# Kernel optimization log

Hardware: AMD Instinct MI355X
Metric: run time of the kernel (lower is better)

The kernel has to match this reference:

```python
import jax, jax.numpy as jnp
import numpy as np

N = 100000   # nodes
E = 640000   # edges (before self-loops)
G = 1000     # graphs in batch
D_IN = 100
D = 128
EPS = 1e-5


def setup_inputs() -> dict:
    key = jax.random.key(0)
    ks = jax.random.split(key, 12)
    x = jax.random.normal(ks[0], (N, D_IN), dtype=jnp.float32)
    edge_index = jax.random.randint(ks[1], (2, E), 0, N, dtype=jnp.int64)
    edge_weight = jax.random.uniform(ks[2], (E,), dtype=jnp.float32)
    batch = jnp.sort(jax.random.randint(ks[3], (N,), 0, G, dtype=jnp.int64))
    def glorot(k, shape):
        fan = shape[0]
        return jax.random.normal(k, shape, dtype=jnp.float32) / np.float32(np.sqrt(fan))
    return {
        "x": x, "edge_index": edge_index, "edge_weight": edge_weight, "batch": batch,
        "W0": glorot(ks[4], (D_IN, D)), "b0": jnp.zeros((D,), jnp.float32),
        "W1": glorot(ks[5], (D, D)),    "b1": jnp.zeros((D,), jnp.float32),
        "W2": glorot(ks[6], (D, D)),    "b2": jnp.zeros((D,), jnp.float32),
        "gamma": jnp.ones((3, D), jnp.float32), "beta": jnp.zeros((3, D), jnp.float32),
        "run_mean": jnp.zeros((3, D), jnp.float32), "run_var": jnp.ones((3, D), jnp.float32),
        "Wout": glorot(ks[7], (D, 1)), "bout": jnp.zeros((1,), jnp.float32),
    }


def reference(x, edge_index, edge_weight, batch, W0, b0, W1, b1, W2, b2,
              gamma, beta, run_mean, run_var, Wout, bout):
    n = x.shape[0]
    # add self-loops with weight 1 (GCNConv default)
    loop = jnp.arange(n, dtype=edge_index.dtype)
    src = jnp.concatenate([edge_index[0], loop])
    dst = jnp.concatenate([edge_index[1], loop])
    ew = jnp.concatenate([edge_weight, jnp.ones((n,), edge_weight.dtype)])
    # symmetric normalization: D^{-1/2} A D^{-1/2}
    deg = jax.ops.segment_sum(ew, dst, num_segments=n)
    dinv = jnp.where(deg > 0, jax.lax.rsqrt(deg), 0.0)
    norm = dinv[src] * ew * dinv[dst]            # [E+N]

    def gcn_bn_relu(h, W, b, g, bt, rm, rv):
        h = h @ W                                 # linear first (cheaper gather dim)
        agg = jax.ops.segment_sum(h[src] * norm[:, None], dst, num_segments=n)
        agg = agg + b
        # BatchNorm1d in eval mode (running stats); dropout is identity in eval
        agg = g * (agg - rm) * jax.lax.rsqrt(rv + EPS) + bt
        return jax.nn.relu(agg)

    h = gcn_bn_relu(x, W0, b0, gamma[0], beta[0], run_mean[0], run_var[0])
    h = gcn_bn_relu(h, W1, b1, gamma[1], beta[1], run_mean[1], run_var[1])
    h = gcn_bn_relu(h, W2, b2, gamma[2], beta[2], run_mean[2], run_var[2])

    # global mean pool over graphs
    counts = jax.ops.segment_sum(jnp.ones((n,), h.dtype), batch, num_segments=G)
    pooled = jax.ops.segment_sum(h, batch, num_segments=G) / jnp.maximum(counts, 1.0)[:, None]
    return pooled @ Wout + bout
```

## Files before the change

### kernel.cpp

```cpp
#include <hip/hip_runtime.h>

#define BN_EPS 1e-5f
#define BINCAP 32

static inline size_t align_up(size_t x, size_t a) { return (x + a - 1) & ~(a - 1); }

typedef __attribute__((ext_vector_type(8))) short bf16x8;
typedef __attribute__((ext_vector_type(4))) float f32x4;

__device__ __forceinline__ void bf16split(float v, unsigned short& hi, unsigned short& lo) {
    unsigned u = __float_as_uint(v);
    unsigned rh = (u + 0x7FFFu + ((u >> 16) & 1u)) >> 16;
    float fh = __uint_as_float(rh << 16);
    hi = (unsigned short)rh;
    float rem = v - fh;
    unsigned u2 = __float_as_uint(rem);
    lo = (unsigned short)((u2 + 0x7FFFu + ((u2 >> 16) & 1u)) >> 16);
}

__device__ __forceinline__ unsigned short bf16rne(float v) {
    unsigned u = __float_as_uint(v);
    return (unsigned short)((u + 0x7FFFu + ((u >> 16) & 1u)) >> 16);
}

__device__ __forceinline__ float bf16f(unsigned h) { return __uint_as_float(h << 16); }
__device__ __forceinline__ float chlo(unsigned u) { return __uint_as_float(u << 16); }
__device__ __forceinline__ float chhi(unsigned u) { return __uint_as_float(u & 0xffff0000u); }


__global__ void place_kernel(const int* __restrict__ src, const int* __restrict__ dst,
                             const float* __restrict__ ew,
                             int* __restrict__ cntc, int2* __restrict__ bins, int E) {
    int e = blockIdx.x * blockDim.x + threadIdx.x;
    if (e >= E) return;
    int d = dst[e];
    int pos = atomicAdd(&cntc[d], 1);
    if (pos < BINCAP)
        bins[(size_t)d * BINCAP + pos] = make_int2(src[e], __float_as_int(ew[e]));
}


__global__ void deginv_kernel(const int* __restrict__ cntc, const int2* __restrict__ bins,
                              float* __restrict__ dinv, int N) {
    int i = blockIdx.x * blockDim.x + threadIdx.x;
    if (i >= N) return;
    int cnt = cntc[i]; if (cnt > BINCAP) cnt = BINCAP;
    const int2* b = bins + (size_t)i * BINCAP;
    float s = 0.f;
    for (int j = 0; j < cnt; ++j) s += __int_as_float(b[j].y);
    dinv[i] = rsqrtf(s + 1.0f);
}


__global__ void normfix_kernel(const int* __restrict__ cntc, int2* __restrict__ bins,
                               const float* __restrict__ dinv, int N) {
    int i = blockIdx.x * blockDim.x + threadIdx.x;
    if (i >= N) return;
    int cnt = cntc[i]; if (cnt > BINCAP) cnt = BINCAP;
    float di = dinv[i];
    int2* b = bins + (size_t)i * BINCAP;
    for (int j = 0; j < cnt; ++j) {
        int2 pr = b[j];
        float w = __int_as_float(pr.y) * dinv[pr.x] * di;
        b[j].y = __float_as_int(w);
    }
}


__global__ void convw_kernel(const float* __restrict__ W0, const float* __restrict__ W1,
                             const float* __restrict__ W2, int K0,
                             unsigned short* __restrict__ Whi, unsigned short* __restrict__ Wlo) {
    int idx = blockIdx.x * blockDim.x + threadIdx.x;
    if (idx >= 3 * 32 * 64 * 8) return;
    int j    = idx & 7;
    int lane = (idx >> 3) & 63;
    int f    = (idx >> 9) & 31;
    int l    = idx >> 14;
    int ct = f >> 2, k0c = f & 3;
    int quad = lane >> 4, m16 = lane & 15;
    int n = ct * 16 + m16;
    int k = k0c * 32 + quad * 8 + j;
    const float* W = (l == 0) ? W0 : (l == 1) ? W1 : W2;
    int Kl = (l == 0) ? K0 : 128;
    float v = (k < Kl) ? W[(size_t)k * 128 + n] : 0.f;
    unsigned short hi, lo;
    bf16split(v, hi, lo);
    Whi[idx] = hi;
    Wlo[idx] = lo;
}


__device__ __forceinline__ void mfma_tail(const bf16x8 ah[4], const bf16x8 al[4],
                                          const unsigned short* __restrict__ Whi,
                                          const unsigned short* __restrict__ Wlo,
                                          unsigned short* __restrict__ Yh,
                                          int row0, int quad, int m16, int lane, int N) {
    const bf16x8* Wh8 = (const bf16x8*)Whi;
    const bf16x8* Wl8 = (const bf16x8*)Wlo;

    f32x4 acc[8];
    #pragma unroll
    for (int ct = 0; ct < 8; ++ct) acc[ct] = (f32x4){0.f, 0.f, 0.f, 0.f};

    bf16x8 bh[2][4], bl[2][4];
    #pragma unroll
    for (int k0c = 0; k0c < 4; ++k0c) {
        bh[0][k0c] = Wh8[k0c * 64 + lane];
        bl[0][k0c] = Wl8[k0c * 64 + lane];
    }

    __builtin_amdgcn_s_setprio(1);
    #pragma unroll
    for (int ct = 0; ct < 8; ++ct) {
        int cur = ct & 1, nxt = cur ^ 1;
        if (ct < 7) {
            #pragma unroll
            for (int k0c = 0; k0c < 4; ++k0c) {
                bh[nxt][k0c] = Wh8[((ct + 1) * 4 + k0c) * 64 + lane];
                bl[nxt][k0c] = Wl8[((ct + 1) * 4 + k0c) * 64 + lane];
            }
        }
        #pragma unroll
        for (int k0c = 0; k0c < 4; ++k0c) {
            acc[ct] = __builtin_amdgcn_mfma_f32_16x16x32_bf16(ah[k0c], bh[cur][k0c], acc[ct], 0, 0, 0);
            acc[ct] = __builtin_amdgcn_mfma_f32_16x16x32_bf16(ah[k0c], bl[cur][k0c], acc[ct], 0, 0, 0);
            acc[ct] = __builtin_amdgcn_mfma_f32_16x16x32_bf16(al[k0c], bh[cur][k0c], acc[ct], 0, 0, 0);
        }
    }
    __builtin_amdgcn_s_setprio(0);

    #pragma unroll
    for (int ct = 0; ct < 8; ++ct) {
        #pragma unroll
        for (int rg = 0; rg < 4; ++rg) {
            int row = row0 + quad * 4 + rg;
            if (row < N)
                Yh[(size_t)row * 128 + ct * 16 + m16] = bf16rne(acc[ct][rg]);
        }
    }
}


__launch_bounds__(256, 2)
__global__ void gemm0_fused_kernel(const float* __restrict__ x, int D_IN,
                                   const unsigned short* __restrict__ Whi,
                                   const unsigned short* __restrict__ Wlo,
                                   unsigned short* __restrict__ Yh, int N) {
    int tid = threadIdx.x;
    int wid = tid >> 6, lane = tid & 63;
    int quad = lane >> 4, m16 = lane & 15;
    int row0 = blockIdx.x * 64 + wid * 16;

    int arow = row0 + m16;
    if (arow > N - 1) arow = N - 1;
    const float* xr = x + (size_t)arow * D_IN;

    bf16x8 ah[4], al[4];
    #pragma unroll
    for (int k0c = 0; k0c < 4; ++k0c) {
        int kb = k0c * 32 + quad * 8;
        float vs[8];
        if (kb + 8 <= D_IN) {
            float4 v0 = *((const float4*)(xr + kb));
            float4 v1 = *((const float4*)(xr + kb + 4));
            vs[0] = v0.x; vs[1] = v0.y; vs[2] = v0.z; vs[3] = v0.w;
            vs[4] = v1.x; vs[5] = v1.y; vs[6] = v1.z; vs[7] = v1.w;
        } else {
            #pragma unroll
            for (int j = 0; j < 8; ++j) vs[j] = (kb + j < D_IN) ? xr[kb + j] : 0.f;
        }
        #pragma unroll
        for (int j = 0; j < 8; ++j) {
            unsigned short hi, lo;
            bf16split(vs[j], hi, lo);
            ah[k0c][j] = (short)hi;
            al[k0c][j] = (short)lo;
        }
    }

    mfma_tail(ah, al, Whi, Wlo, Yh, row0, quad, m16, lane, N);
}


__global__ void scaleshift_kernel(const float* __restrict__ gamma, const float* __restrict__ beta,
                                  const float* __restrict__ rm, const float* __restrict__ rv,
                                  const float* __restrict__ b0, const float* __restrict__ b1,
                                  const float* __restrict__ b2,
                                  float* __restrict__ scale, float* __restrict__ shift) {
    int t = threadIdx.x;
    int l = t >> 7, j = t & 127;
    const float* bs = (l == 0) ? b0 : (l == 1) ? b1 : b2;
    float sc = gamma[t] * rsqrtf(rv[t] + BN_EPS);
    scale[t] = sc;
    shift[t] = beta[t] + (bs[j] - rm[t]) * sc;
}


__device__ __forceinline__ void gather_pair(const unsigned* __restrict__ Yh32,
                                            int2 pr0, int m0, int2 pr1, int m1,
                                            int lane,
                                            float& ax0, float& ay0, float& ax1, float& ay1) {
    int mr0 = (m0 + 7) & ~7, mr1 = (m1 + 7) & ~7;
    int mr = mr0 > mr1 ? mr0 : mr1;
    for (int j = 0; j < mr; j += 8) {
        int a0 = __builtin_amdgcn_readlane(pr0.x, j);
        int a1 = __builtin_amdgcn_readlane(pr0.x, j + 1);
        int a2 = __builtin_amdgcn_readlane(pr0.x, j + 2);
        int a3 = __builtin_amdgcn_readlane(pr0.x, j + 3);
        int a4 = __builtin_amdgcn_readlane(pr0.x, j + 4);
        int a5 = __builtin_amdgcn_readlane(pr0.x, j + 5);
        int a6 = __builtin_amdgcn_readlane(pr0.x, j + 6);
        int a7 = __builtin_amdgcn_readlane(pr0.x, j + 7);
        int b0 = __builtin_amdgcn_readlane(pr1.x, j);
        int b1 = __builtin_amdgcn_readlane(pr1.x, j + 1);
        int b2 = __builtin_amdgcn_readlane(pr1.x, j + 2);
        int b3 = __builtin_amdgcn_readlane(pr1.x, j + 3);
        int b4 = __builtin_amdgcn_readlane(pr1.x, j + 4);
        int b5 = __builtin_amdgcn_readlane(pr1.x, j + 5);
        int b6 = __builtin_amdgcn_readlane(pr1.x, j + 6);
        int b7 = __builtin_amdgcn_readlane(pr1.x, j + 7);
        float wa0 = __int_as_float(__builtin_amdgcn_readlane(pr0.y, j));
        float wa1 = __int_as_float(__builtin_amdgcn_readlane(pr0.y, j + 1));
        float wa2 = __int_as_float(__builtin_amdgcn_readlane(pr0.y, j + 2));
        float wa3 = __int_as_float(__builtin_amdgcn_readlane(pr0.y, j + 3));
        float wa4 = __int_as_float(__builtin_amdgcn_readlane(pr0.y, j + 4));
        float wa5 = __int_as_float(__builtin_amdgcn_readlane(pr0.y, j + 5));
        float wa6 = __int_as_float(__builtin_amdgcn_readlane(pr0.y, j + 6));
        float wa7 = __int_as_float(__builtin_amdgcn_readlane(pr0.y, j + 7));
        float wb0 = __int_as_float(__builtin_amdgcn_readlane(pr1.y, j));
        float wb1 = __int_as_float(__builtin_amdgcn_readlane(pr1.y, j + 1));
        float wb2 = __int_as_float(__builtin_amdgcn_readlane(pr1.y, j + 2));
        float wb3 = __int_as_float(__builtin_amdgcn_readlane(pr1.y, j + 3));
        float wb4 = __int_as_float(__builtin_amdgcn_readlane(pr1.y, j + 4));
        float wb5 = __int_as_float(__builtin_amdgcn_readlane(pr1.y, j + 5));
        float wb6 = __int_as_float(__builtin_amdgcn_readlane(pr1.y, j + 6));
        float wb7 = __int_as_float(__builtin_amdgcn_readlane(pr1.y, j + 7));
        unsigned ua0 = Yh32[(size_t)a0 * 64 + lane];
        unsigned ua1 = Yh32[(size_t)a1 * 64 + lane];
        unsigned ua2 = Yh32[(size_t)a2 * 64 + lane];
        unsigned ua3 = Yh32[(size_t)a3 * 64 + lane];
        unsigned ua4 = Yh32[(size_t)a4 * 64 + lane];
        unsigned ua5 = Yh32[(size_t)a5 * 64 + lane];
        unsigned ua6 = Yh32[(size_t)a6 * 64 + lane];
        unsigned ua7 = Yh32[(size_t)a7 * 64 + lane];
        unsigned ub0 = Yh32[(size_t)b0 * 64 + lane];
        unsigned ub1 = Yh32[(size_t)b1 * 64 + lane];
        unsigned ub2 = Yh32[(size_t)b2 * 64 + lane];
        unsigned ub3 = Yh32[(size_t)b3 * 64 + lane];
        unsigned ub4 = Yh32[(size_t)b4 * 64 + lane];
        unsigned ub5 = Yh32[(size_t)b5 * 64 + lane];
        unsigned ub6 = Yh32[(size_t)b6 * 64 + lane];
        unsigned ub7 = Yh32[(size_t)b7 * 64 + lane];
        ax0 += chlo(ua0) * wa0; ay0 += chhi(ua0) * wa0;
        ax0 += chlo(ua1) * wa1; ay0 += chhi(ua1) * wa1;
        ax0 += chlo(ua2) * wa2; ay0 += chhi(ua2) * wa2;
        ax0 += chlo(ua3) * wa3; ay0 += chhi(ua3) * wa3;
        ax0 += chlo(ua4) * wa4; ay0 += chhi(ua4) * wa4;
        ax0 += chlo(ua5) * wa5; ay0 += chhi(ua5) * wa5;
        ax0 += chlo(ua6) * wa6; ay0 += chhi(ua6) * wa6;
        ax0 += chlo(ua7) * wa7; ay0 += chhi(ua7) * wa7;
        ax1 += chlo(ub0) * wb0; ay1 += chhi(ub0) * wb0;
        ax1 += chlo(ub1) * wb1; ay1 += chhi(ub1) * wb1;
        ax1 += chlo(ub2) * wb2; ay1 += chhi(ub2) * wb2;
        ax1 += chlo(ub3) * wb3; ay1 += chhi(ub3) * wb3;
        ax1 += chlo(ub4) * wb4; ay1 += chhi(ub4) * wb4;
        ax1 += chlo(ub5) * wb5; ay1 += chhi(ub5) * wb5;
        ax1 += chlo(ub6) * wb6; ay1 += chhi(ub6) * wb6;
        ax1 += chlo(ub7) * wb7; ay1 += chhi(ub7) * wb7;
    }
}


__launch_bounds__(64, 4)
__global__ void fused_agg_gemm_kernel(
        const unsigned* __restrict__ Yh_in,
        const int2* __restrict__ bins, const int* __restrict__ cntc,
        const float* __restrict__ dinv,
        const float* __restrict__ scale, const float* __restrict__ shift,
        const unsigned short* __restrict__ Whi, const unsigned short* __restrict__ Wlo,
        unsigned short* __restrict__ Yh_out, int N) {
    __shared__ float sA[16 * 132];
    int lane = threadIdx.x;
    int quad = lane >> 4, m16 = lane & 15;
    int row0 = blockIdx.x * 16;

    float2 sc = ((const float2*)scale)[lane];
    float2 sh = ((const float2*)shift)[lane];

    int mm[16]; float dv[16]; unsigned uh[16]; int2 gg[16];
    #pragma unroll
    for (int i = 0; i < 16; ++i) {
        int n = row0 + i; if (n > N - 1) n = N - 1;
        mm[i] = cntc[n];
        dv[i] = dinv[n];
        uh[i] = Yh_in[(size_t)n * 64 + lane];
    }
    #pragma unroll
    for (int i = 0; i < 16; ++i) {
        int n = row0 + i; if (n > N - 1) n = N - 1;
        int m = mm[i]; if (m > BINCAP) m = BINCAP;
        mm[i] = m;
        gg[i] = (lane < m) ? bins[(size_t)n * BINCAP + lane] : make_int2(n, 0);
    }

    #pragma unroll
    for (int i = 0; i < 16; i += 2) {
        float w00 = dv[i] * dv[i], w01 = dv[i + 1] * dv[i + 1];
        float ax0 = chlo(uh[i]) * w00,     ay0 = chhi(uh[i]) * w00;
        float ax1 = chlo(uh[i + 1]) * w01, ay1 = chhi(uh[i + 1]) * w01;
        gather_pair(Yh_in, gg[i], mm[i], gg[i + 1], mm[i + 1], lane, ax0, ay0, ax1, ay1);
        float ox0 = fmaxf(ax0 * sc.x + sh.x, 0.f);
        float oy0 = fmaxf(ay0 * sc.y + sh.y, 0.f);
        float ox1 = fmaxf(ax1 * sc.x + sh.x, 0.f);
        float oy1 = fmaxf(ay1 * sc.y + sh.y, 0.f);
        *((float2*)&sA[i * 132 + 2 * lane])       = make_float2(ox0, oy0);
        *((float2*)&sA[(i + 1) * 132 + 2 * lane]) = make_float2(ox1, oy1);
    }

    asm volatile("s_waitcnt lgkmcnt(0)" ::: "memory");
    __builtin_amdgcn_sched_barrier(0);

    bf16x8 ah[4], al[4];
    #pragma unroll
    for (int k0c = 0; k0c < 4; ++k0c) {
        float4 v0 = *((const float4*)&sA[m16 * 132 + k0c * 32 + quad * 8]);
        float4 v1 = *((const float4*)&sA[m16 * 132 + k0c * 32 + quad * 8 + 4]);
        float vs[8] = {v0.x, v0.y, v0.z, v0.w, v1.x, v1.y, v1.z, v1.w};
        #pragma unroll
        for (int j = 0; j < 8; ++j) {
            unsigned short hi, lo;
            bf16split(vs[j], hi, lo);
            ah[k0c][j] = (short)hi;
            al[k0c][j] = (short)lo;
        }
    }

    mfma_tail(ah, al, Whi, Wlo, Yh_out, row0, quad, m16, lane, N);
}


__launch_bounds__(256)
__global__ void agg3_kernel(const unsigned* __restrict__ Yh32,
                            const int2* __restrict__ bins, const int* __restrict__ cntc,
                            const float* __restrict__ dinv,
                            const float* __restrict__ scale, const float* __restrict__ shift,
                            const float* __restrict__ Wout,
                            float* __restrict__ snode, int N) {
    int idx = blockIdx.x * blockDim.x + threadIdx.x;
    int pairid = idx >> 6, lane = idx & 63;
    int n0 = pairid * 2;
    if (n0 >= N) return;
    int n1 = n0 + 1; if (n1 > N - 1) n1 = n0;

    int m0 = cntc[n0];
    int m1 = cntc[n1];
    float d0 = dinv[n0], d1 = dinv[n1];
    unsigned uh0 = Yh32[(size_t)n0 * 64 + lane];
    unsigned uh1 = Yh32[(size_t)n1 * 64 + lane];
    if (m0 > BINCAP) m0 = BINCAP;
    if (m1 > BINCAP) m1 = BINCAP;
    int2 pr0 = (lane < m0) ? bins[(size_t)n0 * BINCAP + lane] : make_int2(n0, 0);
    int2 pr1 = (lane < m1) ? bins[(size_t)n1 * BINCAP + lane] : make_int2(n1, 0);

    float w00 = d0 * d0, w01 = d1 * d1;
    float ax0 = chlo(uh0) * w00, ay0 = chhi(uh0) * w00;
    float ax1 = chlo(uh1) * w01, ay1 = chhi(uh1) * w01;
    gather_pair(Yh32, pr0, m0, pr1, m1, lane, ax0, ay0, ax1, ay1);

    float2 sc = ((const float2*)scale)[lane];
    float2 sh = ((const float2*)shift)[lane];
    float2 w  = ((const float2*)Wout)[lane];
    float ox0 = fmaxf(ax0 * sc.x + sh.x, 0.f);
    float oy0 = fmaxf(ay0 * sc.y + sh.y, 0.f);
    float ox1 = fmaxf(ax1 * sc.x + sh.x, 0.f);
    float oy1 = fmaxf(ay1 * sc.y + sh.y, 0.f);
    float s0 = ox0 * w.x + oy0 * w.y;
    float s1 = ox1 * w.x + oy1 * w.y;
    #pragma unroll
    for (int off = 32; off > 0; off >>= 1) {
        s0 += __shfl_down(s0, off, 64);
        s1 += __shfl_down(s1, off, 64);
    }
    if (lane == 0) {
        snode[n0] = s0;
        if (n1 != n0) snode[n1] = s1;
    }
}


__global__ void bounds_kernel(const int* __restrict__ batch, int* __restrict__ gstart,
                              int N, int G) {
    int i = blockIdx.x * blockDim.x + threadIdx.x;
    if (i >= N) return;
    int b = batch[i];
    int prev = (i == 0) ? -1 : batch[i - 1];
    for (int g = prev + 1; g <= b; ++g) gstart[g] = i;
    if (i == N - 1) {
        for (int g = b + 1; g <= G; ++g) gstart[g] = N;
    }
}

__launch_bounds__(256)
__global__ void pool3_kernel(const float* __restrict__ snode, const int* __restrict__ gstart,
                             const float* __restrict__ bout, float* __restrict__ out, int G) {
    int g = blockIdx.x;
    int beg = gstart[g], end = gstart[g + 1];
    int t = threadIdx.x;
    float acc = 0.f;
    for (int n = beg + t; n < end; n += 256) acc += snode[n];
    __shared__ float lds[256];
    lds[t] = acc;
    __syncthreads();
    if (t < 64) lds[t] = lds[t] + lds[t + 64] + lds[t + 128] + lds[t + 192];
    __syncthreads();
    if (t < 64) {
        float s = lds[t];
        #pragma unroll
        for (int off = 32; off > 0; off >>= 1) s += __shfl_down(s, off, 64);
        if (t == 0) {
            float cntf = (float)(end - beg);
            out[g] = s / fmaxf(cntf, 1.0f) + bout[0];
        }
    }
}


extern "C" void kernel_launch(void* const* d_in, const int* in_sizes, int n_in,
                              void* d_out, int out_size, void* d_ws, size_t ws_size,
                              hipStream_t stream) {
    const float* x     = (const float*)d_in[0];
    const int*   ei    = (const int*)d_in[1];
    const float* ew    = (const float*)d_in[2];
    const int*   batch = (const int*)d_in[3];
    const float* W0 = (const float*)d_in[4];
    const float* b0 = (const float*)d_in[5];
    const float* W1 = (const float*)d_in[6];
    const float* b1 = (const float*)d_in[7];
    const float* W2 = (const float*)d_in[8];
    const float* b2 = (const float*)d_in[9];
    const float* gamma = (const float*)d_in[10];
    const float* beta  = (const float*)d_in[11];
    const float* rmean = (const float*)d_in[12];
    const float* rvar  = (const float*)d_in[13];
    const float* Wout  = (const float*)d_in[14];
    const float* bout  = (const float*)d_in[15];

    const int E = in_sizes[2];
    const int N = in_sizes[3];
    const int D_IN = in_sizes[0] / N;
    const int G = out_size;

    const int* src = ei;
    const int* dst = ei + E;

    char* ws = (char*)d_ws;
    size_t off = 0;
    float* dinv  = (float*)(ws + off); off = align_up(off + (size_t)N * 4, 256);
    int* cntc    = (int*)(ws + off);   off = align_up(off + (size_t)N * 4, 256);
    int* gstart  = (int*)(ws + off);   off = align_up(off + ((size_t)G + 1) * 4, 256);
    int2* bins   = (int2*)(ws + off);  off = align_up(off + (size_t)N * BINCAP * 8, 256);
    unsigned short* YAh = (unsigned short*)(ws + off); off = align_up(off + (size_t)N * 128 * 2, 256);
    unsigned short* YBh = (unsigned short*)(ws + off); off = align_up(off + (size_t)N * 128 * 2, 256);
    unsigned short* Whi = (unsigned short*)(ws + off); off = align_up(off + 3 * 16384 * 2, 256);
    unsigned short* Wlo = (unsigned short*)(ws + off); off = align_up(off + 3 * 16384 * 2, 256);
    float* scale = (float*)(ws + off); off = align_up(off + 3 * 128 * 4, 256);
    float* shift = (float*)(ws + off); off = align_up(off + 3 * 128 * 4, 256);
    float* snode = (float*)(ws + off); off = align_up(off + (size_t)N * 4, 256);
    (void)ws_size;

    hipMemsetAsync(cntc, 0, (size_t)N * 4, stream);

    const int tB = 256;
    place_kernel<<<(E + tB - 1) / tB, tB, 0, stream>>>(src, dst, ew, cntc, bins, E);
    deginv_kernel<<<(N + tB - 1) / tB, tB, 0, stream>>>(cntc, bins, dinv, N);
    normfix_kernel<<<(N + tB - 1) / tB, tB, 0, stream>>>(cntc, bins, dinv, N);
    bounds_kernel<<<(N + tB - 1) / tB, tB, 0, stream>>>(batch, gstart, N, G);
    scaleshift_kernel<<<1, 384, 0, stream>>>(gamma, beta, rmean, rvar, b0, b1, b2, scale, shift);
    convw_kernel<<<(3 * 32 * 64 * 8 + tB - 1) / tB, tB, 0, stream>>>(W0, W1, W2, D_IN, Whi, Wlo);

    int gemm0_blocks = (N + 63) / 64;
    int fused_blocks = (N + 15) / 16;

    gemm0_fused_kernel<<<gemm0_blocks, 256, 0, stream>>>(x, D_IN, Whi, Wlo, YAh, N);
    fused_agg_gemm_kernel<<<fused_blocks, 64, 0, stream>>>(
        (const unsigned*)YAh, bins, cntc, dinv,
        scale, shift, Whi + 16384, Wlo + 16384, YBh, N);
    fused_agg_gemm_kernel<<<fused_blocks, 64, 0, stream>>>(
        (const unsigned*)YBh, bins, cntc, dinv,
        scale + 128, shift + 128, Whi + 2 * 16384, Wlo + 2 * 16384, YAh, N);
    {
        long nthread_pair = (long)((N + 1) / 2) * 64;
        int blocks_pair = (int)((nthread_pair + tB - 1) / tB);
        agg3_kernel<<<blocks_pair, tB, 0, stream>>>((const unsigned*)YAh,
            bins, cntc, dinv, scale + 256, shift + 256, Wout, snode, N);
    }

    pool3_kernel<<<G, 256, 0, stream>>>(snode, gstart, bout, (float*)d_out, G);
}
```

Baseline: 318.7 us.

## Merge prep kernels and software-pipeline neighbor gathers in fused aggregation

Combines the weight conversion, BN scale/shift and graph-bounds kernels into one launch to cut launch overhead. In the fused aggregation+GEMM kernel, the first eight neighbor loads plus the self row for the next node pair are issued while the current pair accumulates, double-buffering gathered values to hide memory latency. The extra buffered registers may lower occupancy, and gather_pair is refactored into loops.

```diff
diff --git a/kernel.cpp b/kernel.cpp
--- a/kernel.cpp
+++ b/kernel.cpp
@@ -23,9 +23,9 @@
     return (unsigned short)((u + 0x7FFFu + ((u >> 16) & 1u)) >> 16);
 }
 
-__device__ __forceinline__ float bf16f(unsigned h) { return __uint_as_float(h << 16); }
 __device__ __forceinline__ float chlo(unsigned u) { return __uint_as_float(u << 16); }
 __device__ __forceinline__ float chhi(unsigned u) { return __uint_as_float(u & 0xffff0000u); }
+
 
 
 __global__ void place_kernel(const int* __restrict__ src, const int* __restrict__ dst,
@@ -67,26 +67,50 @@
 }
 
 
-__global__ void convw_kernel(const float* __restrict__ W0, const float* __restrict__ W1,
-                             const float* __restrict__ W2, int K0,
-                             unsigned short* __restrict__ Whi, unsigned short* __restrict__ Wlo) {
+__global__ void prep_kernel(const float* __restrict__ W0, const float* __restrict__ W1,
+                            const float* __restrict__ W2, int K0,
+                            unsigned short* __restrict__ Whi, unsigned short* __restrict__ Wlo,
+                            const float* __restrict__ gamma, const float* __restrict__ beta,
+                            const float* __restrict__ rm, const float* __restrict__ rv,
+                            const float* __restrict__ b0, const float* __restrict__ b1,
+                            const float* __restrict__ b2,
+                            float* __restrict__ scale, float* __restrict__ shift,
+                            const int* __restrict__ batch, int* __restrict__ gstart,
+                            int N, int G) {
     int idx = blockIdx.x * blockDim.x + threadIdx.x;
-    if (idx >= 3 * 32 * 64 * 8) return;
-    int j    = idx & 7;
-    int lane = (idx >> 3) & 63;
-    int f    = (idx >> 9) & 31;
-    int l    = idx >> 14;
-    int ct = f >> 2, k0c = f & 3;
-    int quad = lane >> 4, m16 = lane & 15;
-    int n = ct * 16 + m16;
-    int k = k0c * 32 + quad * 8 + j;
-    const float* W = (l == 0) ? W0 : (l == 1) ? W1 : W2;
-    int Kl = (l == 0) ? K0 : 128;
-    float v = (k < Kl) ? W[(size_t)k * 128 + n] : 0.f;
-    unsigned short hi, lo;
-    bf16split(v, hi, lo);
-    Whi[idx] = hi;
-    Wlo[idx] = lo;
+    if (idx < 3 * 32 * 64 * 8) {
+        int j    = idx & 7;
+        int lane = (idx >> 3) & 63;
+        int f    = (idx >> 9) & 31;
+        int l    = idx >> 14;
+        int ct = f >> 2, k0c = f & 3;
+        int quad = lane >> 4, m16 = lane & 15;
+        int n = ct * 16 + m16;
+        int k = k0c * 32 + quad * 8 + j;
+        const float* W = (l == 0) ? W0 : (l == 1) ? W1 : W2;
+        int Kl = (l == 0) ? K0 : 128;
+        float v = (k < Kl) ? W[(size_t)k * 128 + n] : 0.f;
+        unsigned short hi, lo;
+        bf16split(v, hi, lo);
+        Whi[idx] = hi;
+        Wlo[idx] = lo;
+    } else if (idx < 3 * 32 * 64 * 8 + 384) {
+        int t = idx - 3 * 32 * 64 * 8;
+        int l = t >> 7, j = t & 127;
+        const float* bs = (l == 0) ? b0 : (l == 1) ? b1 : b2;
+        float sc = gamma[t] * rsqrtf(rv[t] + BN_EPS);
+        scale[t] = sc;
+        shift[t] = beta[t] + (bs[j] - rm[t]) * sc;
+    } else {
+        int i = idx - (3 * 32 * 64 * 8 + 384);
+        if (i >= N) return;
+        int b = batch[i];
+        int prev = (i == 0) ? -1 : batch[i - 1];
+        for (int g = prev + 1; g <= b; ++g) gstart[g] = i;
+        if (i == N - 1) {
+            for (int g = b + 1; g <= G; ++g) gstart[g] = N;
+        }
+    }
 }
 
 
@@ -182,20 +206,6 @@
 }
 
 
-__global__ void scaleshift_kernel(const float* __restrict__ gamma, const float* __restrict__ beta,
-                                  const float* __restrict__ rm, const float* __restrict__ rv,
-                                  const float* __restrict__ b0, const float* __restrict__ b1,
-                                  const float* __restrict__ b2,
-                                  float* __restrict__ scale, float* __restrict__ shift) {
-    int t = threadIdx.x;
-    int l = t >> 7, j = t & 127;
-    const float* bs = (l == 0) ? b0 : (l == 1) ? b1 : b2;
-    float sc = gamma[t] * rsqrtf(rv[t] + BN_EPS);
-    scale[t] = sc;
-    shift[t] = beta[t] + (bs[j] - rm[t]) * sc;
-}
-
-
 __device__ __forceinline__ void gather_pair(const unsigned* __restrict__ Yh32,
                                             int2 pr0, int m0, int2 pr1, int m1,
                                             int lane,
@@ -203,70 +213,21 @@
     int mr0 = (m0 + 7) & ~7, mr1 = (m1 + 7) & ~7;
     int mr = mr0 > mr1 ? mr0 : mr1;
     for (int j = 0; j < mr; j += 8) {
-        int a0 = __builtin_amdgcn_readlane(pr0.x, j);
-        int a1 = __builtin_amdgcn_readlane(pr0.x, j + 1);
-        int a2 = __builtin_amdgcn_readlane(pr0.x, j + 2);
-        int a3 = __builtin_amdgcn_readlane(pr0.x, j + 3);
-        int a4 = __builtin_amdgcn_readlane(pr0.x, j + 4);
-        int a5 = __builtin_amdgcn_readlane(pr0.x, j + 5);
-        int a6 = __builtin_amdgcn_readlane(pr0.x, j + 6);
-        int a7 = __builtin_amdgcn_readlane(pr0.x, j + 7);
-        int b0 = __builtin_amdgcn_readlane(pr1.x, j);
-        int b1 = __builtin_amdgcn_readlane(pr1.x, j + 1);
-        int b2 = __builtin_amdgcn_readlane(pr1.x, j + 2);
-        int b3 = __builtin_amdgcn_readlane(pr1.x, j + 3);
-        int b4 = __builtin_amdgcn_readlane(pr1.x, j + 4);
-        int b5 = __builtin_amdgcn_readlane(pr1.x, j + 5);
-        int b6 = __builtin_amdgcn_readlane(pr1.x, j + 6);
-        int b7 = __builtin_amdgcn_readlane(pr1.x, j + 7);
-        float wa0 = __int_as_float(__builtin_amdgcn_readlane(pr0.y, j));
-        float wa1 = __int_as_float(__builtin_amdgcn_readlane(pr0.y, j + 1));
-        float wa2 = __int_as_float(__builtin_amdgcn_readlane(pr0.y, j + 2));
-        float wa3 = __int_as_float(__builtin_amdgcn_readlane(pr0.y, j + 3));
-        float wa4 = __int_as_float(__builtin_amdgcn_readlane(pr0.y, j + 4));
-        float wa5 = __int_as_float(__builtin_amdgcn_readlane(pr0.y, j + 5));
-        float wa6 = __int_as_float(__builtin_amdgcn_readlane(pr0.y, j + 6));
-        float wa7 = __int_as_float(__builtin_amdgcn_readlane(pr0.y, j + 7));
-        float wb0 = __int_as_float(__builtin_amdgcn_readlane(pr1.y, j));
-        float wb1 = __int_as_float(__builtin_amdgcn_readlane(pr1.y, j + 1));
-        float wb2 = __int_as_float(__builtin_amdgcn_readlane(pr1.y, j + 2));
-        float wb3 = __int_as_float(__builtin_amdgcn_readlane(pr1.y, j + 3));
-        float wb4 = __int_as_float(__builtin_amdgcn_readlane(pr1.y, j + 4));
-        float wb5 = __int_as_float(__builtin_amdgcn_readlane(pr1.y, j + 5));
-        float wb6 = __int_as_float(__builtin_amdgcn_readlane(pr1.y, j + 6));
-        float wb7 = __int_as_float(__builtin_amdgcn_readlane(pr1.y, j + 7));
-        unsigned ua0 = Yh32[(size_t)a0 * 64 + lane];
-        unsigned ua1 = Yh32[(size_t)a1 * 64 + lane];
-        unsigned ua2 = Yh32[(size_t)a2 * 64 + lane];
-        unsigned ua3 = Yh32[(size_t)a3 * 64 + lane];
-        unsigned ua4 = Yh32[(size_t)a4 * 64 + lane];
-        unsigned ua5 = Yh32[(size_t)a5 * 64 + lane];
-        unsigned ua6 = Yh32[(size_t)a6 * 64 + lane];
-        unsigned ua7 = Yh32[(size_t)a7 * 64 + lane];
-        unsigned ub0 = Yh32[(size_t)b0 * 64 + lane];
-        unsigned ub1 = Yh32[(size_t)b1 * 64 + lane];
-        unsigned ub2 = Yh32[(size_t)b2 * 64 + lane];
-        unsigned ub3 = Yh32[(size_t)b3 * 64 + lane];
-        unsigned ub4 = Yh32[(size_t)b4 * 64 + lane];
-        unsigned ub5 = Yh32[(size_t)b5 * 64 + lane];
-        unsigned ub6 = Yh32[(size_t)b6 * 64 + lane];
-        unsigned ub7 = Yh32[(size_t)b7 * 64 + lane];
-        ax0 += chlo(ua0) * wa0; ay0 += chhi(ua0) * wa0;
-        ax0 += chlo(ua1) * wa1; ay0 += chhi(ua1) * wa1;
-        ax0 += chlo(ua2) * wa2; ay0 += chhi(ua2) * wa2;
-        ax0 += chlo(ua3) * wa3; ay0 += chhi(ua3) * wa3;
-        ax0 += chlo(ua4) * wa4; ay0 += chhi(ua4) * wa4;
-        ax0 += chlo(ua5) * wa5; ay0 += chhi(ua5) * wa5;
-        ax0 += chlo(ua6) * wa6; ay0 += chhi(ua6) * wa6;
-        ax0 += chlo(ua7) * wa7; ay0 += chhi(ua7) * wa7;
-        ax1 += chlo(ub0) * wb0; ay1 += chhi(ub0) * wb0;
-        ax1 += chlo(ub1) * wb1; ay1 += chhi(ub1) * wb1;
-        ax1 += chlo(ub2) * wb2; ay1 += chhi(ub2) * wb2;
-        ax1 += chlo(ub3) * wb3; ay1 += chhi(ub3) * wb3;
-        ax1 += chlo(ub4) * wb4; ay1 += chhi(ub4) * wb4;
-        ax1 += chlo(ub5) * wb5; ay1 += chhi(ub5) * wb5;
-        ax1 += chlo(ub6) * wb6; ay1 += chhi(ub6) * wb6;
-        ax1 += chlo(ub7) * wb7; ay1 += chhi(ub7) * wb7;
+        unsigned ua[8], ub[8];
+        #pragma unroll
+        for (int t = 0; t < 8; ++t) {
+            int a = __builtin_amdgcn_readlane(pr0.x, j + t);
+            ua[t] = Yh32[(size_t)a * 64 + lane];
+            int b = __builtin_amdgcn_readlane(pr1.x, j + t);
+            ub[t] = Yh32[(size_t)b * 64 + lane];
+        }
+        #pragma unroll
+        for (int t = 0; t < 8; ++t) {
+            float wa = __int_as_float(__builtin_amdgcn_readlane(pr0.y, j + t));
+            ax0 += chlo(ua[t]) * wa; ay0 += chhi(ua[t]) * wa;
+            float wb = __int_as_float(__builtin_amdgcn_readlane(pr1.y, j + t));
+            ax1 += chlo(ub[t]) * wb; ay1 += chhi(ub[t]) * wb;
+        }
     }
 }
 
@@ -287,13 +248,11 @@
     float2 sc = ((const float2*)scale)[lane];
     float2 sh = ((const float2*)shift)[lane];
 
-    int mm[16]; float dv[16]; unsigned uh[16]; int2 gg[16];
+    int mm[16]; int2 gg[16];
     #pragma unroll
     for (int i = 0; i < 16; ++i) {
         int n = row0 + i; if (n > N - 1) n = N - 1;
         mm[i] = cntc[n];
-        dv[i] = dinv[n];
-        uh[i] = Yh_in[(size_t)n * 64 + lane];
     }
     #pragma unroll
     for (int i = 0; i < 16; ++i) {
@@ -303,19 +262,82 @@
         gg[i] = (lane < m) ? bins[(size_t)n * BINCAP + lane] : make_int2(n, 0);
     }
 
-    #pragma unroll
-    for (int i = 0; i < 16; i += 2) {
-        float w00 = dv[i] * dv[i], w01 = dv[i + 1] * dv[i + 1];
-        float ax0 = chlo(uh[i]) * w00,     ay0 = chhi(uh[i]) * w00;
-        float ax1 = chlo(uh[i + 1]) * w01, ay1 = chhi(uh[i + 1]) * w01;
-        gather_pair(Yh_in, gg[i], mm[i], gg[i + 1], mm[i + 1], lane, ax0, ay0, ax1, ay1);
+    unsigned u0[2][8], u1[2][8];
+    unsigned uhb0[2], uhb1[2];
+    float dvb0[2], dvb1[2];
+
+#define ISSUE_PAIR(P, B) do {                                                  \
+        int n0_ = row0 + 2 * (P);     if (n0_ > N - 1) n0_ = N - 1;            \
+        int n1_ = row0 + 2 * (P) + 1; if (n1_ > N - 1) n1_ = N - 1;            \
+        dvb0[B] = dinv[n0_];  dvb1[B] = dinv[n1_];                             \
+        uhb0[B] = Yh_in[(size_t)n0_ * 64 + lane];                              \
+        uhb1[B] = Yh_in[(size_t)n1_ * 64 + lane];                              \
+        _Pragma("unroll")                                                      \
+        for (int t_ = 0; t_ < 8; ++t_) {                                       \
+            int s0_ = __builtin_amdgcn_readlane(gg[2 * (P)].x, t_);            \
+            u0[B][t_] = Yh_in[(size_t)s0_ * 64 + lane];                        \
+            int s1_ = __builtin_amdgcn_readlane(gg[2 * (P) + 1].x, t_);        \
+            u1[B][t_] = Yh_in[(size_t)s1_ * 64 + lane];                        \
+        }                                                                      \
+    } while (0)
+
+    ISSUE_PAIR(0, 0);
+
+    #pragma unroll
+    for (int p = 0; p < 8; ++p) {
+        int cur = p & 1, nxt = cur ^ 1;
+        if (p < 7) ISSUE_PAIR(p + 1, nxt);
+
+        int i0 = 2 * p, i1 = 2 * p + 1;
+        float w00 = dvb0[cur] * dvb0[cur], w01 = dvb1[cur] * dvb1[cur];
+        float ax0 = chlo(uhb0[cur]) * w00, ay0 = chhi(uhb0[cur]) * w00;
+        float ax1 = chlo(uhb1[cur]) * w01, ay1 = chhi(uhb1[cur]) * w01;
+
+        #pragma unroll
+        for (int t = 0; t < 8; ++t) {
+            float wa = __int_as_float(__builtin_amdgcn_readlane(gg[i0].y, t));
+            ax0 += chlo(u0[cur][t]) * wa; ay0 += chhi(u0[cur][t]) * wa;
+            float wb = __int_as_float(__builtin_amdgcn_readlane(gg[i1].y, t));
+            ax1 += chlo(u1[cur][t]) * wb; ay1 += chhi(u1[cur][t]) * wb;
+        }
+
+        int mr0 = (mm[i0] + 7) & ~7;
+        for (int j = 8; j < mr0; j += 8) {
+            unsigned v[8];
+            #pragma unroll
+            for (int t = 0; t < 8; ++t) {
+                int s = __builtin_amdgcn_readlane(gg[i0].x, j + t);
+                v[t] = Yh_in[(size_t)s * 64 + lane];
+            }
+            #pragma unroll
+            for (int t = 0; t < 8; ++t) {
+                float w = __int_as_float(__builtin_amdgcn_readlane(gg[i0].y, j + t));
+                ax0 += chlo(v[t]) * w; ay0 += chhi(v[t]) * w;
+            }
+        }
+        int mr1 = (mm[i1] + 7) & ~7;
+        for (int j = 8; j < mr1; j += 8) {
+            unsigned v[8];
+            #pragma unroll
+            for (int t = 0; t < 8; ++t) {
+                int s = __builtin_amdgcn_readlane(gg[i1].x, j + t);
+                v[t] = Yh_in[(size_t)s * 64 + lane];
+            }
+            #pragma unroll
+            for (int t = 0; t < 8; ++t) {
+                float w = __int_as_float(__builtin_amdgcn_readlane(gg[i1].y, j + t));
+                ax1 += chlo(v[t]) * w; ay1 += chhi(v[t]) * w;
+            }
+        }
+
         float ox0 = fmaxf(ax0 * sc.x + sh.x, 0.f);
         float oy0 = fmaxf(ay0 * sc.y + sh.y, 0.f);
         float ox1 = fmaxf(ax1 * sc.x + sh.x, 0.f);
         float oy1 = fmaxf(ay1 * sc.y + sh.y, 0.f);
-        *((float2*)&sA[i * 132 + 2 * lane])       = make_float2(ox0, oy0);
-        *((float2*)&sA[(i + 1) * 132 + 2 * lane]) = make_float2(ox1, oy1);
-    }
+        *((float2*)&sA[i0 * 132 + 2 * lane]) = make_float2(ox0, oy0);
+        *((float2*)&sA[i1 * 132 + 2 * lane]) = make_float2(ox1, oy1);
+    }
+#undef ISSUE_PAIR
 
     asm volatile("s_waitcnt lgkmcnt(0)" ::: "memory");
     __builtin_amdgcn_sched_barrier(0);
@@ -387,18 +409,6 @@
     }
 }
 
-
-__global__ void bounds_kernel(const int* __restrict__ batch, int* __restrict__ gstart,
-                              int N, int G) {
-    int i = blockIdx.x * blockDim.x + threadIdx.x;
-    if (i >= N) return;
-    int b = batch[i];
-    int prev = (i == 0) ? -1 : batch[i - 1];
-    for (int g = prev + 1; g <= b; ++g) gstart[g] = i;
-    if (i == N - 1) {
-        for (int g = b + 1; g <= G; ++g) gstart[g] = N;
-    }
-}
 
 __launch_bounds__(256)
 __global__ void pool3_kernel(const float* __restrict__ snode, const int* __restrict__ gstart,
@@ -474,9 +484,13 @@
     place_kernel<<<(E + tB - 1) / tB, tB, 0, stream>>>(src, dst, ew, cntc, bins, E);
     deginv_kernel<<<(N + tB - 1) / tB, tB, 0, stream>>>(cntc, bins, dinv, N);
     normfix_kernel<<<(N + tB - 1) / tB, tB, 0, stream>>>(cntc, bins, dinv, N);
-    bounds_kernel<<<(N + tB - 1) / tB, tB, 0, stream>>>(batch, gstart, N, G);
-    scaleshift_kernel<<<1, 384, 0, stream>>>(gamma, beta, rmean, rvar, b0, b1, b2, scale, shift);
-    convw_kernel<<<(3 * 32 * 64 * 8 + tB - 1) / tB, tB, 0, stream>>>(W0, W1, W2, D_IN, Whi, Wlo);
+    {
+        int prep_threads = 3 * 32 * 64 * 8 + 384 + N;
+        prep_kernel<<<(prep_threads + tB - 1) / tB, tB, 0, stream>>>(
+            W0, W1, W2, D_IN, Whi, Wlo,
+            gamma, beta, rmean, rvar, b0, b1, b2, scale, shift,
+            batch, gstart, N, G);
+    }
 
     int gemm0_blocks = (N + 63) / 64;
     int fused_blocks = (N + 15) / 16;
```

After: 309.0 us. 1.03x faster.
